# Kernel optimization log

Measured on AMD Instinct MI355X. Metric: run time of the kernel, lower is better.

The kernel has to match this reference:

```python
import jax, jax.numpy as jnp
import numpy as np

NUM_HEADS = 12

def setup_inputs() -> dict:
    key = jax.random.key(0)
    ks = jax.random.split(key, 6)
    B, N, C = 8, 1024, 768
    x = jax.random.normal(ks[0], (B, N, C), dtype=jnp.float32)
    qkv_w = jax.random.normal(ks[1], (3 * C, C), dtype=jnp.float32) * 0.02
    qkv_b = jax.random.normal(ks[2], (3 * C,), dtype=jnp.float32) * 0.02
    static_a = jax.random.normal(ks[3], (1, NUM_HEADS, N, N), dtype=jnp.float32) * 0.02
    proj_w = jax.random.normal(ks[4], (C, C), dtype=jnp.float32) * 0.02
    proj_b = jax.random.normal(ks[5], (C,), dtype=jnp.float32) * 0.02
    return {"x": x, "qkv_w": qkv_w, "qkv_b": qkv_b, "static_a": static_a,
            "proj_w": proj_w, "proj_b": proj_b}

def reference(x, qkv_w, qkv_b, static_a, proj_w, proj_b):
    B, N, C = x.shape
    H = NUM_HEADS
    D = C // H
    scale = D ** -0.5
    # qkv: [B,N,3C] -> [3,B,H,N,D]
    qkv = (x @ qkv_w.T + qkv_b).reshape(B, N, 3, H, D).transpose(2, 0, 3, 1, 4)
    q, k, v = qkv[0], qkv[1], qkv[2]
    attn = jnp.einsum('bhnd,bhmd->bhnm', q, k) * scale
    attn = jax.nn.softmax(attn, axis=-1)
    attn = attn + static_a  # static bias added AFTER softmax (no renorm)
    out = jnp.einsum('bhnm,bhmd->bhnd', attn, v)  # [B,H,N,D]
    out = out.transpose(0, 2, 1, 3).reshape(B, N, C)
    return out @ proj_w.T + proj_b
```

## Files before the change

kernel.cpp:

```cpp
#include <hip/hip_runtime.h>
#include <math.h>

#define NB   8
#define SEQ  1024
#define CH   768
#define NH   12
#define HD   64
#define BHT  (NB * NH)
#define QKVN 2304

typedef unsigned short u16;
typedef unsigned int   u32;
typedef __attribute__((ext_vector_type(8))) short bf16x8;
typedef __attribute__((ext_vector_type(4))) float f32x4;

__device__ __forceinline__ float bf2f(u32 s) {
    union { u32 u; float f; } v; v.u = s << 16; return v.f;
}
__device__ __forceinline__ u16 f2bf(float f) {
    union { float f; u32 u; } v; v.f = f;
    u32 u = v.u;
    return (u16)((u + 0x7fffu + ((u >> 16) & 1u)) >> 16);
}
__device__ __forceinline__ u32 cvtpk(float lo, float hi) {
    u32 r;
    asm("v_cvt_pk_bf16_f32 %0, %1, %2" : "=v"(r) : "v"(lo), "v"(hi));
    return r;
}
__device__ __forceinline__ float ld1(const u16* p) { return bf2f((u32)*p); }
__device__ __forceinline__ void st1(u16* p, float v) { *p = f2bf(v); }
__device__ __forceinline__ void st4v(u16* p, float a, float b, float c, float d) {
    ushort4 o; o.x = f2bf(a); o.y = f2bf(b); o.z = f2bf(c); o.w = f2bf(d);
    *(ushort4*)p = o;
}
__device__ __forceinline__ void st4v(float* p, float a, float b, float c, float d) {
    float4 o; o.x = a; o.y = b; o.z = c; o.w = d;
    *(float4*)p = o;
}
__device__ __forceinline__ void gload16(const u16* g, u16* l) {
    __builtin_amdgcn_global_load_lds(
        (const __attribute__((address_space(1))) void*)g,
        (__attribute__((address_space(3))) void*)l, 16, 0, 0);
}

__global__ void detect_kernel(const u32* __restrict__ x, int* __restrict__ flag) {
    __shared__ int cnt;
    if (threadIdx.x == 0) cnt = 0;
    __syncthreads();
    int c = 0;
    for (int i = threadIdx.x; i < 2048; i += 256) {
        const u32 e0 = (x[i] >> 7) & 0xFFu;
        c += (e0 >= 110u && e0 <= 132u) ? 1 : 0;
    }
    atomicAdd(&cnt, c);
    __syncthreads();
    if (threadIdx.x == 0) *flag = (cnt > 1024) ? 1 : 0;
}

#define PREP_V4 5309184
__device__ __forceinline__ void prep_seg(size_t v, const size_t e0[6],
                                         int* segp, size_t* offp) {
    int seg = 5;
    if      (v < 1572864) seg = 0;
    else if (v < 2015232) seg = 1;
    else if (v < 2015808) seg = 2;
    else if (v < 5161536) seg = 3;
    else if (v < 5308992) seg = 4;
    *segp = seg; *offp = v * 4 - e0[seg];
}

__global__ __launch_bounds__(256) void prep_all(
    const int* __restrict__ flag,
    const void* __restrict__ s0, const void* __restrict__ s1, const void* __restrict__ s2,
    const void* __restrict__ s3, const void* __restrict__ s4, const void* __restrict__ s5,
    u16* __restrict__ dst)
{
    const size_t e0[6] = {0, 6291456, 8060928, 8063232, 20646144, 21235968};
    if (*flag != 0) {
        const u16* const srcs[6] = {(const u16*)s0, (const u16*)s1, (const u16*)s2,
                                    (const u16*)s3, (const u16*)s4, (const u16*)s5};
        for (size_t v = blockIdx.x * 256 + threadIdx.x; v < PREP_V4; v += (size_t)gridDim.x * 256) {
            int seg; size_t off;
            prep_seg(v, e0, &seg, &off);
            *(ushort4*)(dst + v * 4) = *(const ushort4*)(srcs[seg] + off);
        }
    } else {
        const float* const srcs[6] = {(const float*)s0, (const float*)s1, (const float*)s2,
                                      (const float*)s3, (const float*)s4, (const float*)s5};
        for (size_t v = blockIdx.x * 256 + threadIdx.x; v < PREP_V4; v += (size_t)gridDim.x * 256) {
            int seg; size_t off;
            prep_seg(v, e0, &seg, &off);
            const float4 f = *(const float4*)(srcs[seg] + off);
            ushort4 o; o.x = f2bf(f.x); o.y = f2bf(f.y); o.z = f2bf(f.z); o.w = f2bf(f.w);
            *(ushort4*)(dst + v * 4) = o;
        }
    }
}

template<bool SWAP>
__device__ __forceinline__ void gemm128_core(
    const u16* __restrict__ Ag, const u16* __restrict__ Bg,
    f32x4 acc[4][4], u16* As, u16* Bs, int wm, int wn, int l15, int quad)
{
    const int t = threadIdx.x;
    const int w = t >> 6, lane = t & 63;
    const int lr = lane >> 2, lc = lane & 3;
    const int r0 = w * 16 + lr;
    const int r1 = 64 + w * 16 + lr;
    const int g0 = (lc + r0) & 3, g1 = (lc + r1) & 3;
    const u16* a0 = Ag + (size_t)r0 * CH + g0 * 8;
    const u16* a1 = Ag + (size_t)r1 * CH + g1 * 8;
    const u16* b0 = Bg + (size_t)r0 * CH + g0 * 8;
    const u16* b1 = Bg + (size_t)r1 * CH + g1 * 8;
    u16* lA0 = As + w * 512;
    u16* lA1 = As + 2048 + w * 512;
    u16* lB0 = Bs + w * 512;
    u16* lB1 = Bs + 2048 + w * 512;

#pragma unroll
    for (int mi = 0; mi < 4; mi++)
#pragma unroll
        for (int ni = 0; ni < 4; ni++) { f32x4 z = {0.f,0.f,0.f,0.f}; acc[mi][ni] = z; }

    for (int k0 = 0; k0 < CH; k0 += 32) {
        __syncthreads();
        gload16(a0 + k0, lA0);
        gload16(a1 + k0, lA1);
        gload16(b0 + k0, lB0);
        gload16(b1 + k0, lB1);
        __syncthreads();
        bf16x8 af[4], bfr[4];
#pragma unroll
        for (int mi = 0; mi < 4; mi++) {
            const int ra = wm * 64 + mi * 16 + l15;
            af[mi] = *(const bf16x8*)&As[ra * 32 + ((quad - ra) & 3) * 8];
        }
#pragma unroll
        for (int ni = 0; ni < 4; ni++) {
            const int rb = wn * 64 + ni * 16 + l15;
            bfr[ni] = *(const bf16x8*)&Bs[rb * 32 + ((quad - rb) & 3) * 8];
        }
#pragma unroll
        for (int mi = 0; mi < 4; mi++)
#pragma unroll
            for (int ni = 0; ni < 4; ni++)
                acc[mi][ni] = SWAP
                    ? __builtin_amdgcn_mfma_f32_16x16x32_bf16(bfr[ni], af[mi], acc[mi][ni], 0, 0, 0)
                    : __builtin_amdgcn_mfma_f32_16x16x32_bf16(af[mi], bfr[ni], acc[mi][ni], 0, 0, 0);
    }
}

__global__ __launch_bounds__(256) void qkv_gemm(
    const u16* __restrict__ x, const u16* __restrict__ w, const u16* __restrict__ bias,
    u16* __restrict__ Qn, u16* __restrict__ Kn, u16* __restrict__ Vt)
{
    __shared__ u16 As[128 * 32];
    __shared__ u16 Bs[128 * 32];
    const int t = threadIdx.x, lane = t & 63, wv = t >> 6;
    const int l15 = lane & 15, quad = lane >> 4;
    const int wm = wv >> 1, wn = wv & 1;
    const int m0 = blockIdx.y * 128, n0 = blockIdx.x * 128;
    const int which = n0 / CH;
    const int h     = ((n0 % CH) >> 6) + wn;
    const int b     = m0 >> 10;
    const size_t bh = (size_t)b * NH + h;
    const int sq0   = m0 & 1023;
    f32x4 acc[4][4];

    if (which == 2) {
        gemm128_core<false>(x + (size_t)m0 * CH, w + (size_t)n0 * CH,
                            acc, As, Bs, wm, wn, l15, quad);
        float bv[4];
#pragma unroll
        for (int ni = 0; ni < 4; ni++) bv[ni] = ld1(bias + n0 + wn * 64 + ni * 16 + l15);
#pragma unroll
        for (int mi = 0; mi < 4; mi++) {
            const int seq = sq0 + wm * 64 + mi * 16 + quad * 4;
#pragma unroll
            for (int ni = 0; ni < 4; ni++) {
                const int d = ni * 16 + l15;
                st4v(&Vt[(bh * HD + d) * SEQ + seq],
                     acc[mi][ni][0] + bv[ni], acc[mi][ni][1] + bv[ni],
                     acc[mi][ni][2] + bv[ni], acc[mi][ni][3] + bv[ni]);
            }
        }
    } else {
        gemm128_core<true>(x + (size_t)m0 * CH, w + (size_t)n0 * CH,
                           acc, As, Bs, wm, wn, l15, quad);
        u16* T2 = which ? Kn : Qn;
        const float qsc = which ? 1.0f : 0.18033688011112042f;
        float bvr[4][4];
#pragma unroll
        for (int ni = 0; ni < 4; ni++)
#pragma unroll
            for (int r = 0; r < 4; r++)
                bvr[ni][r] = ld1(bias + n0 + wn * 64 + ni * 16 + quad * 4 + r);
#pragma unroll
        for (int mi = 0; mi < 4; mi++) {
            const int seq = sq0 + wm * 64 + mi * 16 + l15;
#pragma unroll
            for (int ni = 0; ni < 4; ni++) {
                const int dbase = ni * 16 + quad * 4;
                st4v(&T2[(bh * SEQ + seq) * HD + dbase],
                     (acc[mi][ni][0] + bvr[ni][0]) * qsc,
                     (acc[mi][ni][1] + bvr[ni][1]) * qsc,
                     (acc[mi][ni][2] + bvr[ni][2]) * qsc,
                     (acc[mi][ni][3] + bvr[ni][3]) * qsc);
            }
        }
    }
}

__global__ __launch_bounds__(256) void attn_kernel(
    const u16* __restrict__ Qn, const u16* __restrict__ Kn, const u16* __restrict__ Vt,
    const u16* __restrict__ Ab, u16* __restrict__ AO)
{
    __shared__ u16 Ks[64 * 72];
    __shared__ u16 Vs[64 * 72];
    __shared__ u16 Ps[4 * 32 * 72];

    const int qb = blockIdx.x;
    const int y  = blockIdx.y;
    const int hh = y >> 3, b = y & 7;
    const size_t bh = (size_t)b * NH + hh;
    const int t  = threadIdx.x;
    const int w  = t >> 6, lane = t & 63;
    const int l15 = lane & 15, quad = lane >> 4;
    const int sr = t >> 2, sc = (t & 3) * 16;
    const int i0g = qb * 128 + w * 32;
    u16* Psw = Ps + w * 32 * 72;

    bf16x8 qa[2][2];
#pragma unroll
    for (int isub = 0; isub < 2; isub++)
#pragma unroll
        for (int db = 0; db < 2; db++)
            qa[isub][db] = *(const bf16x8*)(Qn +
                (bh * SEQ + i0g + isub * 16 + l15) * HD + db * 32 + quad * 8);

    f32x4 Op[2][4], Oa[2][4];
#pragma unroll
    for (int i = 0; i < 2; i++)
#pragma unroll
        for (int d = 0; d < 4; d++) { f32x4 z = {0.f,0.f,0.f,0.f}; Op[i][d] = z; Oa[i][d] = z; }
    float rl[2][4] = {{0.f,0.f,0.f,0.f},{0.f,0.f,0.f,0.f}};

    for (int kt = 0; kt < 16; kt++) {
        const int j0 = kt * 64;
        bf16x8 afr[2][2];
#pragma unroll
        for (int jb = 0; jb < 2; jb++)
#pragma unroll
            for (int isub = 0; isub < 2; isub++)
                afr[jb][isub] = *(const bf16x8*)(Ab +
                    ((size_t)hh * SEQ + i0g + isub * 16 + l15) * SEQ
                    + j0 + jb * 32 + quad * 8);

        const u16* kp = Kn + (bh * SEQ + j0 + sr) * HD + sc;
        const u16* vp = Vt + (bh * HD + sr) * SEQ + j0 + sc;
        const uint4 k0v = *(const uint4*)kp, k1v = *(const uint4*)(kp + 8);
        const uint4 v0v = *(const uint4*)vp, v1v = *(const uint4*)(vp + 8);
        __syncthreads();
        *(uint4*)&Ks[sr * 72 + sc] = k0v; *(uint4*)&Ks[sr * 72 + sc + 8] = k1v;
        *(uint4*)&Vs[sr * 72 + sc] = v0v; *(uint4*)&Vs[sr * 72 + sc + 8] = v1v;
        __syncthreads();

#pragma unroll
        for (int j16 = 0; j16 < 4; j16++) {
            const bf16x8 kf0 = *(const bf16x8*)&Ks[(j16 * 16 + l15) * 72 + quad * 8];
            const bf16x8 kf1 = *(const bf16x8*)&Ks[(j16 * 16 + l15) * 72 + 32 + quad * 8];
#pragma unroll
            for (int isub = 0; isub < 2; isub++) {
                f32x4 s = {0.f, 0.f, 0.f, 0.f};
                s = __builtin_amdgcn_mfma_f32_16x16x32_bf16(qa[isub][0], kf0, s, 0, 0, 0);
                s = __builtin_amdgcn_mfma_f32_16x16x32_bf16(qa[isub][1], kf1, s, 0, 0, 0);
#pragma unroll
                for (int r = 0; r < 4; r++) {
                    const float p = exp2f(fminf(s[r], 86.6f));
                    rl[isub][r] += p;
                    Psw[(isub * 16 + quad * 4 + r) * 72 + j16 * 16 + l15] = (u16)cvtpk(p, p);
                }
            }
        }

#pragma unroll
        for (int jb = 0; jb < 2; jb++) {
            bf16x8 pf[2];
#pragma unroll
            for (int isub = 0; isub < 2; isub++)
                pf[isub] = *(const bf16x8*)&Psw[(isub * 16 + l15) * 72 + jb * 32 + quad * 8];
#pragma unroll
            for (int d16 = 0; d16 < 4; d16++) {
                const bf16x8 vf = *(const bf16x8*)&Vs[(d16 * 16 + l15) * 72 + jb * 32 + quad * 8];
#pragma unroll
                for (int isub = 0; isub < 2; isub++) {
                    Op[isub][d16] = __builtin_amdgcn_mfma_f32_16x16x32_bf16(vf, pf[isub], Op[isub][d16], 0, 0, 0);
                    Oa[isub][d16] = __builtin_amdgcn_mfma_f32_16x16x32_bf16(vf, afr[jb][isub], Oa[isub][d16], 0, 0, 0);
                }
            }
        }
    }

    float inv[2];
#pragma unroll
    for (int isub = 0; isub < 2; isub++) {
        float rr[4];
#pragma unroll
        for (int r = 0; r < 4; r++) {
            float v = rl[isub][r];
            v += __shfl_xor(v, 1); v += __shfl_xor(v, 2);
            v += __shfl_xor(v, 4); v += __shfl_xor(v, 8);
            rr[r] = v;
        }
        const int src = (l15 >> 2) << 4;
        const float t0 = __shfl(rr[0], src), t1 = __shfl(rr[1], src);
        const float t2 = __shfl(rr[2], src), t3 = __shfl(rr[3], src);
        const float sel = (l15 & 2) ? ((l15 & 1) ? t3 : t2)
                                    : ((l15 & 1) ? t1 : t0);
        inv[isub] = 1.f / sel;
    }
#pragma unroll
    for (int isub = 0; isub < 2; isub++) {
        const int n = i0g + isub * 16 + l15;
#pragma unroll
        for (int d16 = 0; d16 < 4; d16++)
            st4v(&AO[((size_t)b * SEQ + n) * CH + hh * HD + d16 * 16 + quad * 4],
                 Op[isub][d16][0] * inv[isub] + Oa[isub][d16][0],
                 Op[isub][d16][1] * inv[isub] + Oa[isub][d16][1],
                 Op[isub][d16][2] * inv[isub] + Oa[isub][d16][2],
                 Op[isub][d16][3] * inv[isub] + Oa[isub][d16][3]);
    }
}

__global__ __launch_bounds__(256) void proj_all(
    const int* __restrict__ flag,
    const u16* __restrict__ AO, const u16* __restrict__ w, const u16* __restrict__ bias,
    void* __restrict__ outv)
{
    __shared__ u16 As[128 * 32];
    __shared__ u16 Bs[128 * 32];
    const int isbf = *flag;
    const int t = threadIdx.x, lane = t & 63, wv = t >> 6;
    const int l15 = lane & 15, quad = lane >> 4;
    const int wm = wv >> 1, wn = wv & 1;
    const int m0 = blockIdx.y * 128, n0 = blockIdx.x * 128;

    f32x4 acc[4][4];
    gemm128_core<true>(AO + (size_t)m0 * CH, w + (size_t)n0 * CH,
                       acc, As, Bs, wm, wn, l15, quad);

    float bvr[4][4];
#pragma unroll
    for (int ni = 0; ni < 4; ni++)
#pragma unroll
        for (int r = 0; r < 4; r++)
            bvr[ni][r] = ld1(bias + n0 + wn * 64 + ni * 16 + quad * 4 + r);
#pragma unroll
    for (int mi = 0; mi < 4; mi++) {
        const int m = m0 + wm * 64 + mi * 16 + l15;
#pragma unroll
        for (int ni = 0; ni < 4; ni++) {
            const int n = n0 + wn * 64 + ni * 16 + quad * 4;
            if (isbf)
                st4v((u16*)outv + (size_t)m * CH + n,
                     acc[mi][ni][0] + bvr[ni][0], acc[mi][ni][1] + bvr[ni][1],
                     acc[mi][ni][2] + bvr[ni][2], acc[mi][ni][3] + bvr[ni][3]);
            else
                st4v((float*)outv + (size_t)m * CH + n,
                     acc[mi][ni][0] + bvr[ni][0], acc[mi][ni][1] + bvr[ni][1],
                     acc[mi][ni][2] + bvr[ni][2], acc[mi][ni][3] + bvr[ni][3]);
        }
    }
}

extern "C" void kernel_launch(void* const* d_in, const int* in_sizes, int n_in,
                              void* d_out, int out_size, void* d_ws, size_t ws_size,
                              hipStream_t stream) {
    (void)in_sizes; (void)n_in; (void)out_size; (void)ws_size;
    u16* ws = (u16*)d_ws;
    u16* xb   = ws;
    u16* wqb  = ws + 6291456;
    u16* bqb  = ws + 8060928;
    u16* Ab   = ws + 8063232;
    u16* pwb  = ws + 20646144;
    u16* pbb  = ws + 21235968;
    u16* arena_end = ws + 21236736;
    const size_t S1 = (size_t)NB * NH * SEQ * HD;
    u16* Qn = arena_end;
    u16* Kn = Qn + S1;
    u16* Vt = Kn + S1;
    u16* AO = Vt + S1;
    int* flag = (int*)(AO + S1);

    detect_kernel<<<dim3(1), dim3(256), 0, stream>>>((const u32*)d_in[0], flag);

    const dim3 blk(256);
    prep_all<<<dim3(4096), blk, 0, stream>>>(flag,
        d_in[0], d_in[1], d_in[2], d_in[3], d_in[4], d_in[5], ws);

    qkv_gemm<<<dim3(QKVN / 128, (NB * SEQ) / 128), blk, 0, stream>>>(
        xb, wqb, bqb, Qn, Kn, Vt);
    attn_kernel<<<dim3(SEQ / 128, BHT), blk, 0, stream>>>(Qn, Kn, Vt, Ab, AO);

    proj_all<<<dim3(CH / 128, (NB * SEQ) / 128), blk, 0, stream>>>(
        flag, AO, pwb, pbb, d_out);
}
```

Measured before the change: 280.7 us.

## Halve attention query tile per block and switch softmax to natural exp

Each attention workgroup now handles 64 query rows (16 per wave) instead of 128, doubling the grid so more workgroups are in flight, and each wave's register and P-tile footprint is halved. K/V tiles are loaded into LDS twice as often overall, since each K/V block now serves fewer query rows. The exp2 path with the log2e-folded Q scale is replaced by __expf with a plain 0.125 scale, and the P conversion uses a software bf16 round instead of the packed convert instruction. This trades K/V reuse for occupancy and spends more ALU work on the exponent.

New measurement: 279.9 us. No clear change (-0.3%).

```diff
diff --git a/kernel.cpp b/kernel.cpp
--- a/kernel.cpp
+++ b/kernel.cpp
@@ -22,13 +22,7 @@
     u32 u = v.u;
     return (u16)((u + 0x7fffu + ((u >> 16) & 1u)) >> 16);
 }
-__device__ __forceinline__ u32 cvtpk(float lo, float hi) {
-    u32 r;
-    asm("v_cvt_pk_bf16_f32 %0, %1, %2" : "=v"(r) : "v"(lo), "v"(hi));
-    return r;
-}
 __device__ __forceinline__ float ld1(const u16* p) { return bf2f((u32)*p); }
-__device__ __forceinline__ void st1(u16* p, float v) { *p = f2bf(v); }
 __device__ __forceinline__ void st4v(u16* p, float a, float b, float c, float d) {
     ushort4 o; o.x = f2bf(a); o.y = f2bf(b); o.z = f2bf(c); o.w = f2bf(d);
     *(ushort4*)p = o;
@@ -188,7 +182,7 @@
         gemm128_core<true>(x + (size_t)m0 * CH, w + (size_t)n0 * CH,
                            acc, As, Bs, wm, wn, l15, quad);
         u16* T2 = which ? Kn : Qn;
-        const float qsc = which ? 1.0f : 0.18033688011112042f;
+        const float qsc = which ? 1.0f : 0.125f;
         float bvr[4][4];
 #pragma unroll
         for (int ni = 0; ni < 4; ni++)
@@ -217,7 +211,7 @@
 {
     __shared__ u16 Ks[64 * 72];
     __shared__ u16 Vs[64 * 72];
-    __shared__ u16 Ps[4 * 32 * 72];
+    __shared__ u16 Ps[4 * 16 * 72];
 
     const int qb = blockIdx.x;
     const int y  = blockIdx.y;
@@ -227,34 +221,27 @@
     const int w  = t >> 6, lane = t & 63;
     const int l15 = lane & 15, quad = lane >> 4;
     const int sr = t >> 2, sc = (t & 3) * 16;
-    const int i0g = qb * 128 + w * 32;
-    u16* Psw = Ps + w * 32 * 72;
-
-    bf16x8 qa[2][2];
-#pragma unroll
-    for (int isub = 0; isub < 2; isub++)
-#pragma unroll
-        for (int db = 0; db < 2; db++)
-            qa[isub][db] = *(const bf16x8*)(Qn +
-                (bh * SEQ + i0g + isub * 16 + l15) * HD + db * 32 + quad * 8);
-
-    f32x4 Op[2][4], Oa[2][4];
-#pragma unroll
-    for (int i = 0; i < 2; i++)
-#pragma unroll
-        for (int d = 0; d < 4; d++) { f32x4 z = {0.f,0.f,0.f,0.f}; Op[i][d] = z; Oa[i][d] = z; }
-    float rl[2][4] = {{0.f,0.f,0.f,0.f},{0.f,0.f,0.f,0.f}};
+    const int i0g = qb * 64 + w * 16;
+    u16* Psw = Ps + w * 16 * 72;
+
+    bf16x8 qa[2];
+#pragma unroll
+    for (int db = 0; db < 2; db++)
+        qa[db] = *(const bf16x8*)(Qn +
+            (bh * SEQ + i0g + l15) * HD + db * 32 + quad * 8);
+
+    f32x4 Op[4], Oa[4];
+#pragma unroll
+    for (int d = 0; d < 4; d++) { f32x4 z = {0.f,0.f,0.f,0.f}; Op[d] = z; Oa[d] = z; }
+    float rl[4] = {0.f,0.f,0.f,0.f};
 
     for (int kt = 0; kt < 16; kt++) {
         const int j0 = kt * 64;
-        bf16x8 afr[2][2];
+        bf16x8 afr[2];
 #pragma unroll
         for (int jb = 0; jb < 2; jb++)
-#pragma unroll
-            for (int isub = 0; isub < 2; isub++)
-                afr[jb][isub] = *(const bf16x8*)(Ab +
-                    ((size_t)hh * SEQ + i0g + isub * 16 + l15) * SEQ
-                    + j0 + jb * 32 + quad * 8);
+            afr[jb] = *(const bf16x8*)(Ab +
+                ((size_t)hh * SEQ + i0g + l15) * SEQ + j0 + jb * 32 + quad * 8);
 
         const u16* kp = Kn + (bh * SEQ + j0 + sr) * HD + sc;
         const u16* vp = Vt + (bh * HD + sr) * SEQ + j0 + sc;
@@ -269,67 +256,51 @@
         for (int j16 = 0; j16 < 4; j16++) {
             const bf16x8 kf0 = *(const bf16x8*)&Ks[(j16 * 16 + l15) * 72 + quad * 8];
             const bf16x8 kf1 = *(const bf16x8*)&Ks[(j16 * 16 + l15) * 72 + 32 + quad * 8];
-#pragma unroll
-            for (int isub = 0; isub < 2; isub++) {
-                f32x4 s = {0.f, 0.f, 0.f, 0.f};
-                s = __builtin_amdgcn_mfma_f32_16x16x32_bf16(qa[isub][0], kf0, s, 0, 0, 0);
-                s = __builtin_amdgcn_mfma_f32_16x16x32_bf16(qa[isub][1], kf1, s, 0, 0, 0);
-#pragma unroll
-                for (int r = 0; r < 4; r++) {
-                    const float p = exp2f(fminf(s[r], 86.6f));
-                    rl[isub][r] += p;
-                    Psw[(isub * 16 + quad * 4 + r) * 72 + j16 * 16 + l15] = (u16)cvtpk(p, p);
-                }
+            f32x4 s = {0.f, 0.f, 0.f, 0.f};
+            s = __builtin_amdgcn_mfma_f32_16x16x32_bf16(qa[0], kf0, s, 0, 0, 0);
+            s = __builtin_amdgcn_mfma_f32_16x16x32_bf16(qa[1], kf1, s, 0, 0, 0);
+#pragma unroll
+            for (int r = 0; r < 4; r++) {
+                const float p = __expf(fminf(s[r], 60.f));
+                rl[r] += p;
+                Psw[(quad * 4 + r) * 72 + j16 * 16 + l15] = f2bf(p);
             }
         }
 
 #pragma unroll
         for (int jb = 0; jb < 2; jb++) {
-            bf16x8 pf[2];
-#pragma unroll
-            for (int isub = 0; isub < 2; isub++)
-                pf[isub] = *(const bf16x8*)&Psw[(isub * 16 + l15) * 72 + jb * 32 + quad * 8];
+            const bf16x8 pf = *(const bf16x8*)&Psw[l15 * 72 + jb * 32 + quad * 8];
 #pragma unroll
             for (int d16 = 0; d16 < 4; d16++) {
                 const bf16x8 vf = *(const bf16x8*)&Vs[(d16 * 16 + l15) * 72 + jb * 32 + quad * 8];
-#pragma unroll
-                for (int isub = 0; isub < 2; isub++) {
-                    Op[isub][d16] = __builtin_amdgcn_mfma_f32_16x16x32_bf16(vf, pf[isub], Op[isub][d16], 0, 0, 0);
-                    Oa[isub][d16] = __builtin_amdgcn_mfma_f32_16x16x32_bf16(vf, afr[jb][isub], Oa[isub][d16], 0, 0, 0);
-                }
+                Op[d16] = __builtin_amdgcn_mfma_f32_16x16x32_bf16(vf, pf, Op[d16], 0, 0, 0);
+                Oa[d16] = __builtin_amdgcn_mfma_f32_16x16x32_bf16(vf, afr[jb], Oa[d16], 0, 0, 0);
             }
         }
     }
 
-    float inv[2];
-#pragma unroll
-    for (int isub = 0; isub < 2; isub++) {
-        float rr[4];
-#pragma unroll
-        for (int r = 0; r < 4; r++) {
-            float v = rl[isub][r];
-            v += __shfl_xor(v, 1); v += __shfl_xor(v, 2);
-            v += __shfl_xor(v, 4); v += __shfl_xor(v, 8);
-            rr[r] = v;
-        }
-        const int src = (l15 >> 2) << 4;
-        const float t0 = __shfl(rr[0], src), t1 = __shfl(rr[1], src);
-        const float t2 = __shfl(rr[2], src), t3 = __shfl(rr[3], src);
-        const float sel = (l15 & 2) ? ((l15 & 1) ? t3 : t2)
-                                    : ((l15 & 1) ? t1 : t0);
-        inv[isub] = 1.f / sel;
-    }
-#pragma unroll
-    for (int isub = 0; isub < 2; isub++) {
-        const int n = i0g + isub * 16 + l15;
-#pragma unroll
-        for (int d16 = 0; d16 < 4; d16++)
-            st4v(&AO[((size_t)b * SEQ + n) * CH + hh * HD + d16 * 16 + quad * 4],
-                 Op[isub][d16][0] * inv[isub] + Oa[isub][d16][0],
-                 Op[isub][d16][1] * inv[isub] + Oa[isub][d16][1],
-                 Op[isub][d16][2] * inv[isub] + Oa[isub][d16][2],
-                 Op[isub][d16][3] * inv[isub] + Oa[isub][d16][3]);
-    }
+    float rr[4];
+#pragma unroll
+    for (int r = 0; r < 4; r++) {
+        float v = rl[r];
+        v += __shfl_xor(v, 1); v += __shfl_xor(v, 2);
+        v += __shfl_xor(v, 4); v += __shfl_xor(v, 8);
+        rr[r] = v;
+    }
+    const int src = (l15 >> 2) << 4;
+    const float t0 = __shfl(rr[0], src), t1 = __shfl(rr[1], src);
+    const float t2 = __shfl(rr[2], src), t3 = __shfl(rr[3], src);
+    const float sel = (l15 & 2) ? ((l15 & 1) ? t3 : t2)
+                                : ((l15 & 1) ? t1 : t0);
+    const float inv = 1.f / sel;
+    const int n = i0g + l15;
+#pragma unroll
+    for (int d16 = 0; d16 < 4; d16++)
+        st4v(&AO[((size_t)b * SEQ + n) * CH + hh * HD + d16 * 16 + quad * 4],
+             Op[d16][0] * inv + Oa[d16][0],
+             Op[d16][1] * inv + Oa[d16][1],
+             Op[d16][2] * inv + Oa[d16][2],
+             Op[d16][3] * inv + Oa[d16][3]);
 }
 
 __global__ __launch_bounds__(256) void proj_all(
@@ -400,7 +371,7 @@
 
     qkv_gemm<<<dim3(QKVN / 128, (NB * SEQ) / 128), blk, 0, stream>>>(
         xb, wqb, bqb, Qn, Kn, Vt);
-    attn_kernel<<<dim3(SEQ / 128, BHT), blk, 0, stream>>>(Qn, Kn, Vt, Ab, AO);
+    attn_kernel<<<dim3(SEQ / 64, BHT), blk, 0, stream>>>(Qn, Kn, Vt, Ab, AO);
 
     proj_all<<<dim3(CH / 128, (NB * SEQ) / 128), blk, 0, stream>>>(
         flag, AO, pwb, pbb, d_out);
```
